# Performance work log

Measured on AMD Instinct MI355X. Metric: run time of the kernel, lower is better.

## Reference

```python
import jax, jax.numpy as jnp
import numpy as np

B, N, C = 4, 1024, 1024
H = 16
D = C // H  # 64
HID = int(int(C * 4.0) * 2 / 3)  # 2730
EPS = 1e-6


def rmsnorm(x, w):
    return x * jax.lax.rsqrt(jnp.mean(x * x, axis=-1, keepdims=True) + EPS) * w


def rope_cos_sin(n, d):
    inv_freq = 1.0 / (10000.0 ** (jnp.arange(0, d, 2, dtype=jnp.float32) / d))
    t = jnp.arange(n, dtype=jnp.float32)
    freqs = jnp.einsum('i,j->ij', t, inv_freq)  # [N, D/2]
    emb = jnp.concatenate([freqs, freqs], axis=-1)  # [N, D]
    return jnp.cos(emb), jnp.sin(emb)


def rotate_half(x):
    x1, x2 = jnp.split(x, 2, axis=-1)
    return jnp.concatenate([-x2, x1], axis=-1)


def setup_inputs() -> dict:
    key = jax.random.key(0)
    ks = jax.random.split(key, 12)
    s = lambda fan_in: 1.0 / np.sqrt(fan_in)
    return {
        'x': jax.random.normal(ks[0], (B, N, C), jnp.float32),
        'c': jax.random.normal(ks[1], (B, C), jnp.float32),
        'norm1_w': jnp.ones((C,), jnp.float32),
        'norm2_w': jnp.ones((C,), jnp.float32),
        'qkv_w': jax.random.normal(ks[2], (C, 3 * C), jnp.float32) * s(C),
        'proj_w': jax.random.normal(ks[3], (C, C), jnp.float32) * s(C),
        'proj_b': jnp.zeros((C,), jnp.float32),
        'qn_w': jnp.ones((D,), jnp.float32),
        'kn_w': jnp.ones((D,), jnp.float32),
        'w1': jax.random.normal(ks[4], (C, HID), jnp.float32) * s(C),
        'w2': jax.random.normal(ks[5], (HID, C), jnp.float32) * s(HID),
        'w3': jax.random.normal(ks[6], (C, HID), jnp.float32) * s(C),
        'ada_w': jax.random.normal(ks[7], (C, 6 * C), jnp.float32) * s(C),
        'ada_b': jnp.zeros((6 * C,), jnp.float32),
    }


def reference(x, c, norm1_w, norm2_w, qkv_w, proj_w, proj_b, qn_w, kn_w, w1, w2, w3, ada_w, ada_b):
    # AdaLN modulation params from conditioning
    mods = jax.nn.silu(c) @ ada_w + ada_b  # [B, 6C]
    sh_msa, sc_msa, g_msa, sh_mlp, sc_mlp, g_mlp = jnp.split(mods, 6, axis=-1)

    # --- attention branch ---
    x_mod = rmsnorm(x, norm1_w) * (1 + sc_msa[:, None, :]) + sh_msa[:, None, :]
    qkv = (x_mod @ qkv_w).reshape(B, N, 3, H, D).transpose(2, 0, 3, 1, 4)  # [3,B,H,N,D]
    q, k, v = qkv[0], qkv[1], qkv[2]
    q = rmsnorm(q, qn_w)
    k = rmsnorm(k, kn_w)
    cos, sin = rope_cos_sin(N, D)  # [N, D]
    q = q * cos + rotate_half(q) * sin
    k = k * cos + rotate_half(k) * sin
    attn = jax.nn.softmax(jnp.einsum('bhqd,bhkd->bhqk', q, k) * (D ** -0.5), axis=-1)
    o = jnp.einsum('bhqk,bhkd->bhqd', attn, v).transpose(0, 2, 1, 3).reshape(B, N, C)
    x = x + g_msa[:, None, :] * (o @ proj_w + proj_b)

    # --- SwiGLU MLP branch ---
    x_mod = rmsnorm(x, norm2_w) * (1 + sc_mlp[:, None, :]) + sh_mlp[:, None, :]
    mlp = (jax.nn.silu(x_mod @ w1) * (x_mod @ w3)) @ w2
    x = x + g_mlp[:, None, :] * mlp
    return x
```

## Files before the change

kernel.cpp:

```cpp
#include <hip/hip_runtime.h>
#include <hip/hip_bf16.h>
#include <stdint.h>

using bf16 = __hip_bfloat16;
using bf16x8 = __attribute__((ext_vector_type(8))) short;
using f32x4  = __attribute__((ext_vector_type(4))) float;
using short4v = __attribute__((ext_vector_type(4))) short;

#define EPSF 1e-6f

__device__ __forceinline__ unsigned short f2bu(float x) {
  union { bf16 h; unsigned short u; } cvt;
  cvt.h = __float2bfloat16(x);
  return cvt.u;
}

typedef __attribute__((address_space(3))) void as3_void;
typedef const __attribute__((address_space(1))) void as1_void;

__device__ __forceinline__ void gload_lds16(const void* g, void* l) {
  as1_void* gp = (as1_void*)(uintptr_t)g;
  as3_void* lp = (as3_void*)(uint32_t)(uintptr_t)l;
  __builtin_amdgcn_global_load_lds(gp, lp, 16, 0, 0);
}

__global__ void rope_tab(float* __restrict__ cosT, float* __restrict__ sinT) {
  const int i = blockIdx.x * 256 + threadIdx.x;
  const int n = i >> 5, fi = i & 31;
  const float invf = powf(10000.f, -(float)fi * (1.f / 32.f));
  const float ang = (float)n * invf;
  cosT[i] = cosf(ang);
  sinT[i] = sinf(ang);
}

__global__ void __launch_bounds__(256) ada_part(const float* __restrict__ cc,
                                                const float* __restrict__ adaw,
                                                float* __restrict__ part) {
  __shared__ float sc[256];
  __shared__ float red[1024];
  const int t = threadIdx.x;
  const int cb = blockIdx.x % 48, ks = blockIdx.x / 48;
  const int k0 = ks * 64;
  {
    const int b = t >> 6, kk = t & 63;
    const float v = cc[b * 1024 + k0 + kk];
    sc[t] = v / (1.f + __expf(-v));
  }
  __syncthreads();
  const int colL = t & 127, kh = t >> 7;
  const int col = cb * 128 + colL;
  float a0 = 0.f, a1 = 0.f, a2 = 0.f, a3 = 0.f;
  const float* ap = adaw + (size_t)(k0 + kh * 32) * 6144 + col;
#pragma unroll
  for (int k = 0; k < 32; ++k) {
    const float awv = ap[(size_t)k * 6144];
    const int kk = kh * 32 + k;
    a0 += sc[kk] * awv; a1 += sc[64 + kk] * awv;
    a2 += sc[128 + kk] * awv; a3 += sc[192 + kk] * awv;
  }
  red[kh * 512 + 0 * 128 + colL] = a0;
  red[kh * 512 + 1 * 128 + colL] = a1;
  red[kh * 512 + 2 * 128 + colL] = a2;
  red[kh * 512 + 3 * 128 + colL] = a3;
  __syncthreads();
  if (kh == 0) {
#pragma unroll
    for (int b = 0; b < 4; ++b) {
      const float s = red[b * 128 + colL] + red[512 + b * 128 + colL];
      part[(size_t)(ks * 4 + b) * 6144 + col] = s;
    }
  }
}

__global__ void __launch_bounds__(256) ada_reduce(const float* __restrict__ part,
                                                  const float* __restrict__ adab,
                                                  float* __restrict__ mods) {
  const int i = blockIdx.x * 256 + threadIdx.x;
  const int b = i / 6144, col = i % 6144;
  float s = adab[col];
#pragma unroll
  for (int ks = 0; ks < 16; ++ks) s += part[(size_t)(ks * 4 + b) * 6144 + col];
  mods[b * 6144 + col] = s;
}

__global__ void __launch_bounds__(256) norm_mod(const float* __restrict__ X,
                                                const float* __restrict__ wgt,
                                                const float* __restrict__ mods,
                                                int sh_off, int sc_off,
                                                bf16* __restrict__ Y) {
  __shared__ float red[4];
  const int row = blockIdx.x, t = threadIdx.x, l = t & 63, wv = t >> 6;
  const float4 xv = ((const float4*)(X + (size_t)row * 1024))[t];
  float ss = xv.x * xv.x + xv.y * xv.y + xv.z * xv.z + xv.w * xv.w;
#pragma unroll
  for (int off = 1; off < 64; off <<= 1) ss += __shfl_xor(ss, off);
  if (l == 0) red[wv] = ss;
  __syncthreads();
  ss = (red[0] + red[1]) + (red[2] + red[3]);
  const float rs = rsqrtf(ss * (1.f / 1024.f) + EPSF);
  const int b = row >> 10;
  const float* mb = mods + b * 6144;
  const int c0 = t * 4;
  float vals[4] = {xv.x, xv.y, xv.z, xv.w};
  short4v yv;
#pragma unroll
  for (int j = 0; j < 4; j++) {
    const int cc = c0 + j;
    const float y = vals[j] * rs * wgt[cc] * (1.f + mb[sc_off + cc]) + mb[sh_off + cc];
    yv[j] = (short)f2bu(y);
  }
  *(short4v*)(Y + (size_t)row * 1024 + c0) = yv;
}

__global__ void __launch_bounds__(256) transpose_all(const float* __restrict__ qkvw,
                                                     const float* __restrict__ projw,
                                                     const float* __restrict__ w1,
                                                     const float* __restrict__ w3,
                                                     const float* __restrict__ w2,
                                                     bf16* __restrict__ qkvwt,
                                                     bf16* __restrict__ projwt,
                                                     bf16* __restrict__ w1t,
                                                     bf16* __restrict__ w3t,
                                                     bf16* __restrict__ w2t) {
  int id = blockIdx.x;
  const float* src; bf16* dst; int R, Cc, ldd, nbx;
  if (id < 3072)      { src = qkvw;  dst = qkvwt;  R = 1024; Cc = 3072; ldd = 1024; nbx = 96; }
  else if ((id -= 3072) < 1024) { src = projw; dst = projwt; R = 1024; Cc = 1024; ldd = 1024; nbx = 32; }
  else if ((id -= 1024) < 2752) { src = w1;    dst = w1t;    R = 1024; Cc = 2730; ldd = 1024; nbx = 86; }
  else if ((id -= 2752) < 2752) { src = w3;    dst = w3t;    R = 1024; Cc = 2730; ldd = 1024; nbx = 86; }
  else                { id -= 2752; src = w2;    dst = w2t;    R = 2730; Cc = 1024; ldd = 2816; nbx = 32; }
  const int bx = id % nbx, by = id / nbx;
  __shared__ float tile[32][33];
  const int tx = threadIdx.x & 31, ty = threadIdx.x >> 5;
  const int ct = bx * 32, rt = by * 32;
#pragma unroll
  for (int kk = 0; kk < 4; ++kk) {
    const int r = rt + ty + kk * 8;
    float v = 0.f;
    if (r < R && (ct + tx) < Cc) v = src[(size_t)r * Cc + ct + tx];
    tile[ty + kk * 8][tx] = v;
  }
  __syncthreads();
#pragma unroll
  for (int kk = 0; kk < 4; ++kk) {
    const int c = ct + ty + kk * 8;
    const int r = rt + tx;
    if (c < Cc && r < ldd) dst[(size_t)c * ldd + r] = __float2bfloat16(tile[tx][ty + kk * 8]);
  }
}

template <int TN, int EPI>
__global__ void __launch_bounds__(256, 3) gemm_p(const bf16* __restrict__ A, int lda,
                                                 const bf16* __restrict__ Bt, int ldb,
                                                 int K, int Nreal, int ldc,
                                                 bf16* __restrict__ outb,
                                                 float* __restrict__ outf,
                                                 const float* __restrict__ resid,
                                                 const float* __restrict__ gate,
                                                 const float* __restrict__ bias) {
  constexpr int BUFSZ = 8192 + TN * 64;
  constexpr int WN = (TN == 128) ? 2 : 1;
  constexpr int MI = (TN == 128) ? 4 : 2;
  constexpr int WTM = (TN == 128) ? 64 : 32;
  __shared__ char smB[3 * BUFSZ];
  const int t = threadIdx.x, l = t & 63, w = t >> 6;
  const int g = l >> 4, cl = l & 15;
  const int cpx = gridDim.x >> 3;
  const int wg = blockIdx.x;
  const int swz0 = (wg & 7) * cpx + (wg >> 3);
  const int m0 = (swz0 & 31) * 128, n0 = (swz0 >> 5) * TN;
  const int wm = w / WN, wn = w % WN;
  f32x4 acc[MI][4] = {};
  const int NK = K >> 5;
  const int srow = t >> 2;
  const int scol = (((t & 3) ^ ((t >> 3) & 3))) * 8;
  const int rsw = (cl >> 1) & 3;

  auto stage = [&](int kt, int buf) {
    char* dst = smB + buf * BUFSZ;
    const int kk = kt * 32 + scol;
    gload_lds16(A + (size_t)(m0 + srow) * lda + kk,      dst + t * 16);
    gload_lds16(A + (size_t)(m0 + 64 + srow) * lda + kk, dst + 4096 + t * 16);
    gload_lds16(Bt + (size_t)(n0 + srow) * ldb + kk,     dst + 8192 + t * 16);
    if constexpr (TN == 128)
      gload_lds16(Bt + (size_t)(n0 + 64 + srow) * ldb + kk, dst + 12288 + t * 16);
  };

  stage(0, 0);
  stage(1, 1);
  if constexpr (TN == 128) asm volatile("s_waitcnt vmcnt(4)" ::: "memory");
  else                     asm volatile("s_waitcnt vmcnt(3)" ::: "memory");
  __builtin_amdgcn_s_barrier();
  __builtin_amdgcn_sched_barrier(0);
  int cur = 0;
  for (int kt = 0; kt < NK; ++kt) {
    if (kt + 2 < NK) stage(kt + 2, (cur >= 1) ? cur - 1 : 2);
    const bf16* Ab = (const bf16*)(smB + cur * BUFSZ);
    const bf16* Bb = (const bf16*)(smB + cur * BUFSZ + 8192);
    bf16x8 af[MI], bfr[4];
#pragma unroll
    for (int i = 0; i < MI; i++)
      af[i] = *(const bf16x8*)&Ab[(wm * WTM + i * 16 + cl) * 32 + ((g ^ rsw) << 3)];
#pragma unroll
    for (int i = 0; i < 4; i++)
      bfr[i] = *(const bf16x8*)&Bb[(wn * 64 + i * 16 + cl) * 32 + ((g ^ rsw) << 3)];
    __builtin_amdgcn_s_setprio(1);
#pragma unroll
    for (int mi = 0; mi < MI; mi++)
#pragma unroll
      for (int ni = 0; ni < 4; ni++)
        acc[mi][ni] = __builtin_amdgcn_mfma_f32_16x16x32_bf16(af[mi], bfr[ni], acc[mi][ni], 0, 0, 0);
    __builtin_amdgcn_s_setprio(0);
    if (kt + 2 < NK) {
      if constexpr (TN == 128) asm volatile("s_waitcnt vmcnt(4)" ::: "memory");
      else                     asm volatile("s_waitcnt vmcnt(3)" ::: "memory");
    } else {
      asm volatile("s_waitcnt vmcnt(0)" ::: "memory");
    }
    __builtin_amdgcn_s_barrier();
    __builtin_amdgcn_sched_barrier(0);
    cur = (cur + 1 == 3) ? 0 : cur + 1;
  }
#pragma unroll
  for (int mi = 0; mi < MI; mi++) {
#pragma unroll
    for (int ni = 0; ni < 4; ni++) {
      const int c = n0 + wn * 64 + ni * 16 + cl;
#pragma unroll
      for (int j = 0; j < 4; j++) {
        const int r = m0 + wm * WTM + mi * 16 + g * 4 + j;
        const float v = acc[mi][ni][j];
        if constexpr (EPI == 0) {
          if (c < Nreal) outb[(size_t)r * ldc + c] = __float2bfloat16(v);
        } else if constexpr (EPI == 1) {
          const int b = r >> 10;
          outf[(size_t)r * ldc + c] = resid[(size_t)r * ldc + c] + gate[b * 6144 + c] * (v + bias[c]);
        } else if constexpr (EPI == 4) {
          const int b = r >> 10;
          outf[(size_t)r * ldc + c] = resid[(size_t)r * ldc + c] + gate[b * 6144 + c] * v;
        }
      }
    }
  }
}

__global__ void __launch_bounds__(256, 2) gemm_dual(const bf16* __restrict__ A, int lda,
                                                    const bf16* __restrict__ B1t,
                                                    const bf16* __restrict__ B3t, int ldb,
                                                    int K, int Nreal, int ldc,
                                                    bf16* __restrict__ outb) {
  constexpr int BUFSZ = 24576;
  __shared__ char smB[2 * BUFSZ];
  const int t = threadIdx.x, l = t & 63, w = t >> 6;
  const int g = l >> 4, cl = l & 15;
  const int cpx = gridDim.x >> 3;
  const int wg = blockIdx.x;
  const int swz0 = (wg & 7) * cpx + (wg >> 3);
  const int m0 = (swz0 & 31) * 128, n0 = (swz0 >> 5) * 128;
  const int wm = w >> 1, wn = w & 1;
  f32x4 acc1[4][4] = {}, acc3[4][4] = {};
  const int NK = K >> 5;
  const int srow = t >> 2;
  const int scol = (((t & 3) ^ ((t >> 3) & 3))) * 8;
  const int rsw = (cl >> 1) & 3;

  auto stage = [&](int kt, int buf) {
    char* dst = smB + buf * BUFSZ;
    const int kk = kt * 32 + scol;
    gload_lds16(A   + (size_t)(m0 + srow) * lda + kk,      dst + t * 16);
    gload_lds16(A   + (size_t)(m0 + 64 + srow) * lda + kk, dst + 4096 + t * 16);
    gload_lds16(B1t + (size_t)(n0 + srow) * ldb + kk,      dst + 8192 + t * 16);
    gload_lds16(B1t + (size_t)(n0 + 64 + srow) * ldb + kk, dst + 12288 + t * 16);
    gload_lds16(B3t + (size_t)(n0 + srow) * ldb + kk,      dst + 16384 + t * 16);
    gload_lds16(B3t + (size_t)(n0 + 64 + srow) * ldb + kk, dst + 20480 + t * 16);
  };

  stage(0, 0);
  for (int kt = 0; kt < NK; ++kt) {
    if (kt + 1 < NK) {
      stage(kt + 1, (kt + 1) & 1);
      asm volatile("s_waitcnt vmcnt(6)" ::: "memory");
    } else {
      asm volatile("s_waitcnt vmcnt(0)" ::: "memory");
    }
    __builtin_amdgcn_s_barrier();
    __builtin_amdgcn_sched_barrier(0);
    const bf16* Ab  = (const bf16*)(smB + (kt & 1) * BUFSZ);
    const bf16* B1b = (const bf16*)(smB + (kt & 1) * BUFSZ + 8192);
    const bf16* B3b = (const bf16*)(smB + (kt & 1) * BUFSZ + 16384);
    bf16x8 af[4], b1r[4], b3r[4];
#pragma unroll
    for (int i = 0; i < 4; i++)
      af[i] = *(const bf16x8*)&Ab[(wm * 64 + i * 16 + cl) * 32 + ((g ^ rsw) << 3)];
#pragma unroll
    for (int i = 0; i < 4; i++) {
      b1r[i] = *(const bf16x8*)&B1b[(wn * 64 + i * 16 + cl) * 32 + ((g ^ rsw) << 3)];
      b3r[i] = *(const bf16x8*)&B3b[(wn * 64 + i * 16 + cl) * 32 + ((g ^ rsw) << 3)];
    }
    __builtin_amdgcn_s_setprio(1);
#pragma unroll
    for (int mi = 0; mi < 4; mi++)
#pragma unroll
      for (int ni = 0; ni < 4; ni++) {
        acc1[mi][ni] = __builtin_amdgcn_mfma_f32_16x16x32_bf16(af[mi], b1r[ni], acc1[mi][ni], 0, 0, 0);
        acc3[mi][ni] = __builtin_amdgcn_mfma_f32_16x16x32_bf16(af[mi], b3r[ni], acc3[mi][ni], 0, 0, 0);
      }
    __builtin_amdgcn_s_setprio(0);
    __builtin_amdgcn_s_barrier();
    __builtin_amdgcn_sched_barrier(0);
  }
#pragma unroll
  for (int mi = 0; mi < 4; mi++) {
#pragma unroll
    for (int ni = 0; ni < 4; ni++) {
      const int c = n0 + wn * 64 + ni * 16 + cl;
#pragma unroll
      for (int j = 0; j < 4; j++) {
        const int r = m0 + wm * 64 + mi * 16 + g * 4 + j;
        if (c < Nreal) {
          const float hv = acc1[mi][ni][j];
          const float sl = hv / (1.f + __expf(-hv));
          outb[(size_t)r * ldc + c] = __float2bfloat16(sl * acc3[mi][ni][j]);
        } else {
          outb[(size_t)r * ldc + c] = __float2bfloat16(0.f);
        }
      }
    }
  }
}

__global__ void __launch_bounds__(256) qkv_post(const bf16* __restrict__ qkv,
                                                const float* __restrict__ cosT,
                                                const float* __restrict__ sinT,
                                                const float* __restrict__ qnw,
                                                const float* __restrict__ knw,
                                                bf16* __restrict__ Qo, bf16* __restrict__ Ko) {
  const int t = threadIdx.x, l = t & 63, wv = t >> 6;
  const int row = blockIdx.x * 4 + wv;
  const int token = row >> 4, h = row & 15;
  const int b = token >> 10, n = token & 1023;
  const int d = l;
  const bf16* base = qkv + (size_t)token * 3072 + h * 64 + d;
  float q = __bfloat162float(base[0]);
  float k = __bfloat162float(base[1024]);
  float sq = q * q, sk = k * k;
#pragma unroll
  for (int off = 1; off < 64; off <<= 1) {
    sq += __shfl_xor(sq, off);
    sk += __shfl_xor(sk, off);
  }
  q *= rsqrtf(sq * (1.f / 64.f) + EPSF) * qnw[d];
  k *= rsqrtf(sk * (1.f / 64.f) + EPSF) * knw[d];
  const float cs = cosT[n * 32 + (d & 31)];
  const float sn = sinT[n * 32 + (d & 31)];
  const float qx = __shfl_xor(q, 32), kx = __shfl_xor(k, 32);
  const float sgn = (d < 32) ? -1.f : 1.f;
  const float qo = (q * cs + sgn * qx * sn) * 0.125f;
  const float ko = k * cs + sgn * kx * sn;
  const size_t ob = ((size_t)(b * 16 + h) * 1024 + n) * 64 + d;
  Qo[ob] = __float2bfloat16(qo);
  Ko[ob] = __float2bfloat16(ko);
}

__global__ void __launch_bounds__(256) vtrans(const bf16* __restrict__ qkv,
                                              bf16* __restrict__ vbt) {
  __shared__ unsigned short tile[64 * 64];
  const int t = threadIdx.x;
  const int bh = blockIdx.y, nt = blockIdx.x;
  const int b = bh >> 4, h = bh & 15;
  const int n0 = nt * 64;
#pragma unroll
  for (int rep = 0; rep < 2; ++rep) {
    const int ci = t + rep * 256;
    const int r = ci >> 3, dc = ci & 7;
    const bf16x8 v = *(const bf16x8*)(qkv + (size_t)(b * 1024 + n0 + r) * 3072 + 2048 + h * 64 + dc * 8);
#pragma unroll
    for (int j = 0; j < 8; ++j) {
      const int d = dc * 8 + j;
      const int chunk = (r >> 3) ^ (d & 7) ^ ((d >> 3) & 7);
      tile[d * 64 + chunk * 8 + (r & 7)] = (unsigned short)v[j];
    }
  }
  __syncthreads();
#pragma unroll
  for (int rep = 0; rep < 2; ++rep) {
    const int ci = t + rep * 256;
    const int d = ci >> 3, nc = ci & 7;
    const int phys = nc ^ (d & 7) ^ ((d >> 3) & 7);
    const bf16x8 v = *(const bf16x8*)&tile[d * 64 + phys * 8];
    *(bf16x8*)(vbt + (size_t)bh * 65536 + (size_t)d * 1024 + n0 + nc * 8) = v;
  }
}

__global__ void __launch_bounds__(512) attn_fwd(const bf16* __restrict__ Qb,
                                                const bf16* __restrict__ Kb,
                                                const bf16* __restrict__ Vb,
                                                bf16* __restrict__ Ob) {
  __shared__ char KsB[2 * 8192];
  __shared__ char VsB[2 * 8192];
  __shared__ unsigned short Ps[8 * 16 * 64];
  const int t = threadIdx.x, l = t & 63, w = t >> 6;
  const int g = l >> 4, cl = l & 15;
  const int wg = blockIdx.x;
  const int bh = wg & 63;
  const int q0 = (wg >> 6) * 128;
  const bf16* Qg = Qb + (size_t)bh * 65536;
  const bf16* Kg = Kb + (size_t)bh * 65536;
  const bf16* Vg = Vb + (size_t)bh * 65536;
  const int qrow = q0 + w * 16 + cl;
  const bf16x8 aq0 = *(const bf16x8*)(Qg + (size_t)qrow * 64 + g * 8);
  const bf16x8 aq1 = *(const bf16x8*)(Qg + (size_t)qrow * 64 + 32 + g * 8);
  float mreg = -1e30f, lreg = 0.f;
  f32x4 o[4] = {};
  const int kr_l = t >> 3;
  const int ku = (t & 7) ^ ((t >> 3) & 7);
  unsigned short* Pw = Ps + w * 1024;
  const int sxor = cl & 7;

  auto stageKV = [&](int kvt, int buf) {
    const int kv0 = kvt * 64;
    gload_lds16(Kg + (size_t)(kv0 + kr_l) * 64 + ku * 8, KsB + buf * 8192 + w * 1024);
    gload_lds16(Vg + (size_t)kr_l * 1024 + kv0 + ku * 8, VsB + buf * 8192 + w * 1024);
  };

  stageKV(0, 0);
  for (int kvt = 0; kvt < 16; ++kvt) {
    const int cb = kvt & 1;
    if (kvt + 1 < 16) {
      stageKV(kvt + 1, cb ^ 1);
      asm volatile("s_waitcnt vmcnt(2)" ::: "memory");
    } else {
      asm volatile("s_waitcnt vmcnt(0)" ::: "memory");
    }
    __builtin_amdgcn_s_barrier();
    __builtin_amdgcn_sched_barrier(0);
    const char* Kt = KsB + cb * 8192;
    const char* Vt = VsB + cb * 8192;
    f32x4 s[4] = {};
#pragma unroll
    for (int ch = 0; ch < 4; ch++) {
      const int rb = (16 * ch + cl) << 7;
      const bf16x8 bk0 = *(const bf16x8*)(Kt + rb + ((g ^ sxor) << 4));
      s[ch] = __builtin_amdgcn_mfma_f32_16x16x32_bf16(bk0, aq0, s[ch], 0, 0, 0);
      const bf16x8 bk1 = *(const bf16x8*)(Kt + rb + (((4 + g) ^ sxor) << 4));
      s[ch] = __builtin_amdgcn_mfma_f32_16x16x32_bf16(bk1, aq1, s[ch], 0, 0, 0);
    }
    float pm = fmaxf(fmaxf(fmaxf(s[0][0], s[0][1]), fmaxf(s[0][2], s[0][3])),
                     fmaxf(fmaxf(s[1][0], s[1][1]), fmaxf(s[1][2], s[1][3])));
    pm = fmaxf(pm, fmaxf(fmaxf(fmaxf(s[2][0], s[2][1]), fmaxf(s[2][2], s[2][3])),
                         fmaxf(fmaxf(s[3][0], s[3][1]), fmaxf(s[3][2], s[3][3]))));
    pm = fmaxf(pm, __shfl_xor(pm, 16));
    pm = fmaxf(pm, __shfl_xor(pm, 32));
    const float nm = fmaxf(mreg, pm);
    const float al = __expf(mreg - nm);
    mreg = nm;
    float rs = 0.f;
#pragma unroll
    for (int ch = 0; ch < 4; ch++) {
      const float p0 = __expf(s[ch][0] - nm);
      const float p1 = __expf(s[ch][1] - nm);
      const float p2 = __expf(s[ch][2] - nm);
      const float p3 = __expf(s[ch][3] - nm);
      rs += (p0 + p1) + (p2 + p3);
      short4v pk;
      pk[0] = (short)f2bu(p0); pk[1] = (short)f2bu(p1);
      pk[2] = (short)f2bu(p2); pk[3] = (short)f2bu(p3);
      const int phys = (2 * ch + (g >> 1)) ^ sxor;
      *(short4v*)&Pw[cl * 64 + phys * 8 + 4 * (g & 1)] = pk;
    }
    rs += __shfl_xor(rs, 16);
    rs += __shfl_xor(rs, 32);
    lreg = lreg * al + rs;
#pragma unroll
    for (int dc = 0; dc < 4; dc++) {
      o[dc][0] *= al; o[dc][1] *= al; o[dc][2] *= al; o[dc][3] *= al;
    }
    const bf16x8 pa0 = *(const bf16x8*)&Pw[cl * 64 + ((g ^ sxor) << 3)];
    const bf16x8 pa1 = *(const bf16x8*)&Pw[cl * 64 + (((4 + g) ^ sxor) << 3)];
#pragma unroll
    for (int dc = 0; dc < 4; dc++) {
      const int vr = (16 * dc + cl) << 7;
      const bf16x8 bv0 = *(const bf16x8*)(Vt + vr + ((g ^ sxor) << 4));
      o[dc] = __builtin_amdgcn_mfma_f32_16x16x32_bf16(bv0, pa0, o[dc], 0, 0, 0);
      const bf16x8 bv1 = *(const bf16x8*)(Vt + vr + (((4 + g) ^ sxor) << 4));
      o[dc] = __builtin_amdgcn_mfma_f32_16x16x32_bf16(bv1, pa1, o[dc], 0, 0, 0);
    }
    __builtin_amdgcn_s_barrier();
  }
  const int b = bh >> 4, h = bh & 15;
  const float inv = 1.f / lreg;
  const int q = q0 + w * 16 + cl;
  const size_t base = ((size_t)(b * 1024 + q) * 16 + h) * 64;
#pragma unroll
  for (int dc = 0; dc < 4; dc++) {
    short4v ov;
    ov[0] = (short)f2bu(o[dc][0] * inv);
    ov[1] = (short)f2bu(o[dc][1] * inv);
    ov[2] = (short)f2bu(o[dc][2] * inv);
    ov[3] = (short)f2bu(o[dc][3] * inv);
    *(short4v*)(Ob + base + 16 * dc + 4 * g) = ov;
  }
}

extern "C" void kernel_launch(void* const* d_in, const int* in_sizes, int n_in,
                              void* d_out, int out_size, void* d_ws, size_t ws_size,
                              hipStream_t stream) {
  const float* x     = (const float*)d_in[0];
  const float* c     = (const float*)d_in[1];
  const float* n1w   = (const float*)d_in[2];
  const float* n2w   = (const float*)d_in[3];
  const float* qkvw  = (const float*)d_in[4];
  const float* projw = (const float*)d_in[5];
  const float* projb = (const float*)d_in[6];
  const float* qnw   = (const float*)d_in[7];
  const float* knw   = (const float*)d_in[8];
  const float* w1    = (const float*)d_in[9];
  const float* w2    = (const float*)d_in[10];
  const float* w3    = (const float*)d_in[11];
  const float* adaw  = (const float*)d_in[12];
  const float* adab  = (const float*)d_in[13];
  float* outp = (float*)d_out;
  char* ws = (char*)d_ws;
  if (ws_size < 93159424u) return;

  float* ropeC = (float*)(ws + 0);
  float* ropeS = (float*)(ws + 131072);
  float* mods  = (float*)(ws + 262144);
  bf16* xmod   = (bf16*)(ws + 360448);
  bf16* qkvwt  = (bf16*)(ws + 8749056);
  bf16* projwt = (bf16*)(ws + 15040512);
  bf16* w1t    = (bf16*)(ws + 17137664);
  bf16* w3t    = (bf16*)(ws + 22904832);
  bf16* w2t    = (bf16*)(ws + 28672000);
  bf16* qkv    = (bf16*)(ws + 34439168);
  float* apart = (float*)(ws + 34439168);
  bf16* qb     = (bf16*)(ws + 59604992);
  bf16* gbuf   = (bf16*)(ws + 59604992);
  bf16* kb     = (bf16*)(ws + 67993600);
  bf16* vbt    = (bf16*)(ws + 76382208);
  bf16* ob     = (bf16*)(ws + 84770816);

  rope_tab<<<128, 256, 0, stream>>>(ropeC, ropeS);
  ada_part<<<768, 256, 0, stream>>>(c, adaw, apart);
  ada_reduce<<<96, 256, 0, stream>>>(apart, adab, mods);
  transpose_all<<<12416, 256, 0, stream>>>(qkvw, projw, w1, w3, w2,
                                           qkvwt, projwt, w1t, w3t, w2t);

  norm_mod<<<4096, 256, 0, stream>>>(x, n1w, mods, 0, 1024, xmod);
  gemm_p<128, 0><<<768, 256, 0, stream>>>(xmod, 1024, qkvwt, 1024, 1024, 3072, 3072,
                                          qkv, nullptr, nullptr, nullptr, nullptr);
  vtrans<<<dim3(16, 64), 256, 0, stream>>>(qkv, vbt);
  qkv_post<<<16384, 256, 0, stream>>>(qkv, ropeC, ropeS, qnw, knw, qb, kb);
  attn_fwd<<<512, 512, 0, stream>>>(qb, kb, vbt, ob);
  gemm_p<64, 1><<<512, 256, 0, stream>>>(ob, 1024, projwt, 1024, 1024, 1024, 1024,
                                         nullptr, outp, x, mods + 2048, projb);

  norm_mod<<<4096, 256, 0, stream>>>(outp, n2w, mods, 3072, 4096, xmod);
  gemm_dual<<<704, 256, 0, stream>>>(xmod, 1024, w1t, w3t, 1024, 1024, 2730, 2816,
                                     gbuf);
  gemm_p<64, 4><<<512, 256, 0, stream>>>(gbuf, 2816, w2t, 2816, 2816, 1024, 1024,
                                         nullptr, outp, outp, mods + 5120, nullptr);
}
```

Baseline: 248.4 us.

## Fuse QK RMSNorm, RoPE and V transpose into QKV GEMM epilogue

Adds a dedicated QKV GEMM with a triple-buffered LDS pipeline whose epilogue applies per-head RMSNorm and RoPE to Q/K and writes V directly in transposed layout. This removes the intermediate qkv buffer write and the separate qkv_post and vtrans kernels with their extra global reads and launches. The tradeoff is a heavier epilogue with shuffles and scattered 2-byte and 8-byte stores, plus extra LDS traffic to stage the cos/sin tables.

```diff
diff --git a/kernel.cpp b/kernel.cpp
--- a/kernel.cpp
+++ b/kernel.cpp
@@ -244,6 +244,138 @@
   }
 }
 
+__global__ void __launch_bounds__(256, 3) gemm_qkv(const bf16* __restrict__ A, int lda,
+                                                   const bf16* __restrict__ Bt, int ldb,
+                                                   const float* __restrict__ cosT,
+                                                   const float* __restrict__ sinT,
+                                                   const float* __restrict__ qnw,
+                                                   const float* __restrict__ knw,
+                                                   bf16* __restrict__ Qo,
+                                                   bf16* __restrict__ Ko,
+                                                   bf16* __restrict__ vbt) {
+  constexpr int BUFSZ = 16384;
+  __shared__ char smB[3 * BUFSZ];
+  const int t = threadIdx.x, l = t & 63, w = t >> 6;
+  const int g = l >> 4, cl = l & 15;
+  const int cpx = gridDim.x >> 3;
+  const int wg = blockIdx.x;
+  const int swz0 = (wg & 7) * cpx + (wg >> 3);
+  const int m0 = (swz0 & 31) * 128, n0 = (swz0 >> 5) * 128;
+  const int wm = w >> 1, wn = w & 1;
+  f32x4 acc[4][4] = {};
+  const int srow = t >> 2;
+  const int scol = (((t & 3) ^ ((t >> 3) & 3))) * 8;
+  const int rsw = (cl >> 1) & 3;
+
+  auto stage = [&](int kt, int buf) {
+    char* dst = smB + buf * BUFSZ;
+    const int kk = kt * 32 + scol;
+    gload_lds16(A + (size_t)(m0 + srow) * lda + kk,       dst + t * 16);
+    gload_lds16(A + (size_t)(m0 + 64 + srow) * lda + kk,  dst + 4096 + t * 16);
+    gload_lds16(Bt + (size_t)(n0 + srow) * ldb + kk,      dst + 8192 + t * 16);
+    gload_lds16(Bt + (size_t)(n0 + 64 + srow) * ldb + kk, dst + 12288 + t * 16);
+  };
+
+  stage(0, 0);
+  stage(1, 1);
+  asm volatile("s_waitcnt vmcnt(4)" ::: "memory");
+  __builtin_amdgcn_s_barrier();
+  __builtin_amdgcn_sched_barrier(0);
+  int cur = 0;
+  for (int kt = 0; kt < 32; ++kt) {
+    if (kt + 2 < 32) stage(kt + 2, (cur >= 1) ? cur - 1 : 2);
+    const bf16* Ab = (const bf16*)(smB + cur * BUFSZ);
+    const bf16* Bb = (const bf16*)(smB + cur * BUFSZ + 8192);
+    bf16x8 af[4], bfr[4];
+#pragma unroll
+    for (int i = 0; i < 4; i++)
+      af[i] = *(const bf16x8*)&Ab[(wm * 64 + i * 16 + cl) * 32 + ((g ^ rsw) << 3)];
+#pragma unroll
+    for (int i = 0; i < 4; i++)
+      bfr[i] = *(const bf16x8*)&Bb[(wn * 64 + i * 16 + cl) * 32 + ((g ^ rsw) << 3)];
+    __builtin_amdgcn_s_setprio(1);
+#pragma unroll
+    for (int mi = 0; mi < 4; mi++)
+#pragma unroll
+      for (int ni = 0; ni < 4; ni++)
+        acc[mi][ni] = __builtin_amdgcn_mfma_f32_16x16x32_bf16(af[mi], bfr[ni], acc[mi][ni], 0, 0, 0);
+    __builtin_amdgcn_s_setprio(0);
+    if (kt + 2 < 32) asm volatile("s_waitcnt vmcnt(4)" ::: "memory");
+    else             asm volatile("s_waitcnt vmcnt(0)" ::: "memory");
+    __builtin_amdgcn_s_barrier();
+    __builtin_amdgcn_sched_barrier(0);
+    cur = (cur + 1 == 3) ? 0 : cur + 1;
+  }
+
+  float* cosS = (float*)smB;
+  float* sinS = (float*)(smB + 16384);
+  const int nb0 = m0 & 1023;
+  for (int i = t; i < 4096; i += 256) {
+    cosS[i] = cosT[(nb0 + (i >> 5)) * 32 + (i & 31)];
+    sinS[i] = sinT[(nb0 + (i >> 5)) * 32 + (i & 31)];
+  }
+  __syncthreads();
+
+  const int hb = n0 + wn * 64;
+  const int type = hb >> 10;
+  const int h = (hb & 1023) >> 6;
+  const int b = m0 >> 10;
+  const int bh = b * 16 + h;
+
+  if (type == 2) {
+#pragma unroll
+    for (int mi = 0; mi < 4; mi++) {
+      const int r0 = m0 + wm * 64 + mi * 16 + g * 4;
+      const int nn0 = r0 & 1023;
+#pragma unroll
+      for (int ni = 0; ni < 4; ni++) {
+        const int d = ni * 16 + cl;
+        short4v pv;
+#pragma unroll
+        for (int j = 0; j < 4; j++) pv[j] = (short)f2bu(acc[mi][ni][j]);
+        *(short4v*)(vbt + (size_t)bh * 65536 + (size_t)d * 1024 + nn0) = pv;
+      }
+    }
+  } else {
+    bf16* dst = (type == 0) ? Qo : Ko;
+    const float* nwp = (type == 0) ? qnw : knw;
+    const float scale = (type == 0) ? 0.125f : 1.f;
+    float wv[4];
+#pragma unroll
+    for (int ni = 0; ni < 4; ni++) wv[ni] = nwp[ni * 16 + cl];
+#pragma unroll
+    for (int mi = 0; mi < 4; mi++) {
+#pragma unroll
+      for (int j = 0; j < 4; j++) {
+        float ssq = 0.f;
+#pragma unroll
+        for (int ni = 0; ni < 4; ni++) ssq += acc[mi][ni][j] * acc[mi][ni][j];
+        ssq += __shfl_xor(ssq, 1);
+        ssq += __shfl_xor(ssq, 2);
+        ssq += __shfl_xor(ssq, 4);
+        ssq += __shfl_xor(ssq, 8);
+        const float rsn = rsqrtf(ssq * (1.f / 64.f) + EPSF);
+        const int r = m0 + wm * 64 + mi * 16 + g * 4 + j;
+        const int nn = r & 1023, rr = r - m0;
+        float vn[4];
+#pragma unroll
+        for (int ni = 0; ni < 4; ni++) vn[ni] = acc[mi][ni][j] * rsn * wv[ni];
+        const float cs0 = cosS[rr * 32 + cl],      sn0 = sinS[rr * 32 + cl];
+        const float cs1 = cosS[rr * 32 + 16 + cl], sn1 = sinS[rr * 32 + 16 + cl];
+        const float o0 = (vn[0] * cs0 - vn[2] * sn0) * scale;
+        const float o1 = (vn[1] * cs1 - vn[3] * sn1) * scale;
+        const float o2 = (vn[2] * cs0 + vn[0] * sn0) * scale;
+        const float o3 = (vn[3] * cs1 + vn[1] * sn1) * scale;
+        const size_t base = ((size_t)bh * 1024 + nn) * 64;
+        dst[base + cl] = __float2bfloat16(o0);
+        dst[base + 16 + cl] = __float2bfloat16(o1);
+        dst[base + 32 + cl] = __float2bfloat16(o2);
+        dst[base + 48 + cl] = __float2bfloat16(o3);
+      }
+    }
+  }
+}
+
 __global__ void __launch_bounds__(256, 2) gemm_dual(const bf16* __restrict__ A, int lda,
                                                     const bf16* __restrict__ B1t,
                                                     const bf16* __restrict__ B3t, int ldb,
@@ -326,69 +458,6 @@
         }
       }
     }
-  }
-}
-
-__global__ void __launch_bounds__(256) qkv_post(const bf16* __restrict__ qkv,
-                                                const float* __restrict__ cosT,
-                                                const float* __restrict__ sinT,
-                                                const float* __restrict__ qnw,
-                                                const float* __restrict__ knw,
-                                                bf16* __restrict__ Qo, bf16* __restrict__ Ko) {
-  const int t = threadIdx.x, l = t & 63, wv = t >> 6;
-  const int row = blockIdx.x * 4 + wv;
-  const int token = row >> 4, h = row & 15;
-  const int b = token >> 10, n = token & 1023;
-  const int d = l;
-  const bf16* base = qkv + (size_t)token * 3072 + h * 64 + d;
-  float q = __bfloat162float(base[0]);
-  float k = __bfloat162float(base[1024]);
-  float sq = q * q, sk = k * k;
-#pragma unroll
-  for (int off = 1; off < 64; off <<= 1) {
-    sq += __shfl_xor(sq, off);
-    sk += __shfl_xor(sk, off);
-  }
-  q *= rsqrtf(sq * (1.f / 64.f) + EPSF) * qnw[d];
-  k *= rsqrtf(sk * (1.f / 64.f) + EPSF) * knw[d];
-  const float cs = cosT[n * 32 + (d & 31)];
-  const float sn = sinT[n * 32 + (d & 31)];
-  const float qx = __shfl_xor(q, 32), kx = __shfl_xor(k, 32);
-  const float sgn = (d < 32) ? -1.f : 1.f;
-  const float qo = (q * cs + sgn * qx * sn) * 0.125f;
-  const float ko = k * cs + sgn * kx * sn;
-  const size_t ob = ((size_t)(b * 16 + h) * 1024 + n) * 64 + d;
-  Qo[ob] = __float2bfloat16(qo);
-  Ko[ob] = __float2bfloat16(ko);
-}
-
-__global__ void __launch_bounds__(256) vtrans(const bf16* __restrict__ qkv,
-                                              bf16* __restrict__ vbt) {
-  __shared__ unsigned short tile[64 * 64];
-  const int t = threadIdx.x;
-  const int bh = blockIdx.y, nt = blockIdx.x;
-  const int b = bh >> 4, h = bh & 15;
-  const int n0 = nt * 64;
-#pragma unroll
-  for (int rep = 0; rep < 2; ++rep) {
-    const int ci = t + rep * 256;
-    const int r = ci >> 3, dc = ci & 7;
-    const bf16x8 v = *(const bf16x8*)(qkv + (size_t)(b * 1024 + n0 + r) * 3072 + 2048 + h * 64 + dc * 8);
-#pragma unroll
-    for (int j = 0; j < 8; ++j) {
-      const int d = dc * 8 + j;
-      const int chunk = (r >> 3) ^ (d & 7) ^ ((d >> 3) & 7);
-      tile[d * 64 + chunk * 8 + (r & 7)] = (unsigned short)v[j];
-    }
-  }
-  __syncthreads();
-#pragma unroll
-  for (int rep = 0; rep < 2; ++rep) {
-    const int ci = t + rep * 256;
-    const int d = ci >> 3, nc = ci & 7;
-    const int phys = nc ^ (d & 7) ^ ((d >> 3) & 7);
-    const bf16x8 v = *(const bf16x8*)&tile[d * 64 + phys * 8];
-    *(bf16x8*)(vbt + (size_t)bh * 65536 + (size_t)d * 1024 + n0 + nc * 8) = v;
   }
 }
 
@@ -532,7 +601,6 @@
   bf16* w1t    = (bf16*)(ws + 17137664);
   bf16* w3t    = (bf16*)(ws + 22904832);
   bf16* w2t    = (bf16*)(ws + 28672000);
-  bf16* qkv    = (bf16*)(ws + 34439168);
   float* apart = (float*)(ws + 34439168);
   bf16* qb     = (bf16*)(ws + 59604992);
   bf16* gbuf   = (bf16*)(ws + 59604992);
@@ -547,10 +615,8 @@
                                            qkvwt, projwt, w1t, w3t, w2t);
 
   norm_mod<<<4096, 256, 0, stream>>>(x, n1w, mods, 0, 1024, xmod);
-  gemm_p<128, 0><<<768, 256, 0, stream>>>(xmod, 1024, qkvwt, 1024, 1024, 3072, 3072,
-                                          qkv, nullptr, nullptr, nullptr, nullptr);
-  vtrans<<<dim3(16, 64), 256, 0, stream>>>(qkv, vbt);
-  qkv_post<<<16384, 256, 0, stream>>>(qkv, ropeC, ropeS, qnw, knw, qb, kb);
+  gemm_qkv<<<768, 256, 0, stream>>>(xmod, 1024, qkvwt, 1024, ropeC, ropeS, qnw, knw,
+                                    qb, kb, vbt);
   attn_fwd<<<512, 512, 0, stream>>>(qb, kb, vbt, ob);
   gemm_p<64, 1><<<512, 256, 0, stream>>>(ob, 1024, projwt, 1024, 1024, 1024, 1024,
                                          nullptr, outp, x, mods + 2048, projb);
```

Result: faster. 233.9 us (-5.8%).
